# Kernel tuning notes

Hardware: AMD Instinct MI355X
Metric: run time of the kernel (lower is better)

The kernel has to match this reference:

```python
import jax, jax.numpy as jnp
import numpy as np

B, N, D = 512, 100000, 256
MAX_K = 20
EPS = 1e-12


def setup_inputs() -> dict:
    key = jax.random.key(0)
    k1, k2, k3, k4 = jax.random.split(key, 4)
    z_ego = jax.random.normal(k1, (B, D), dtype=jnp.float32)
    exo_bank = jax.random.normal(k2, (N, D), dtype=jnp.float32)
    sim_vt = jax.random.uniform(k3, (B, N), dtype=jnp.float32)
    W = jax.random.normal(k4, (D, D), dtype=jnp.float32) / np.sqrt(D)
    return {"z_ego": z_ego, "exo_bank": exo_bank, "sim_vt": sim_vt, "W": W, "k": 16}


def _l2_normalize(x):
    # matches torch F.normalize semantics with eps clamp
    n = jnp.sqrt(jnp.sum(x * x, axis=-1, keepdims=True))
    return x / jnp.maximum(n, EPS)


def reference(z_ego, exo_bank, sim_vt, W, k):
    # bilinear projection into query space (Linear, no bias)
    q = z_ego @ W.T                              # [B, D]
    k_eff = min(int(k), MAX_K, exo_bank.shape[0])
    # pairwise cosine similarity query x bank
    sim_vv = _l2_normalize(q) @ _l2_normalize(exo_bank).T   # [B, N]
    # combined score (sim_vt already [B, N]; broadcast is identity)
    score = 0.5 * sim_vv + 0.5 * sim_vt          # [B, N]
    _, topk_idx = jax.lax.top_k(score, k_eff)    # [B, k_eff]
    gathered = exo_bank[topk_idx]                # [B, k_eff, D]
    return gathered, topk_idx
```

## Files before the change

### kernel.cpp

```cpp
#include <hip/hip_runtime.h>
#include <math.h>
#include <stdint.h>

#define B_Q    512
#define N_BANK 100000
#define D_DIM  256
#define K16    16

#define NSL2   256
#define NCHUNK 1563
#define TROW   264
#define CHUNK_USHORT (64 * TROW)
#define CHUNK_BYTES  (CHUNK_USHORT * 2)
#define NGRP   6250
#define GSTRIDE 6272
#define MARGIN 5e-3f
#define CAPG   384

#define OFF_QN     0
#define OFF_QNT    0x80000
#define OFF_INORM  0x100000
#define OFF_TH     0x170000
#define OFF_GMAX   0x400000
#define OFF_BANKT  0x1400000
#define WS_NEED    ((size_t)OFF_BANKT + (size_t)NCHUNK * CHUNK_BYTES)

#define FB_OFF_INORM (B_Q * D_DIM * 4)
#define FB_OFF_PSC   (1024 * 1024)
#define FB_OFF_PID   (FB_OFF_PSC + B_Q * 128 * K16 * 4)

typedef __attribute__((ext_vector_type(8))) short short8;
typedef __attribute__((ext_vector_type(4))) float floatx4;

typedef __attribute__((address_space(1))) const unsigned char gu8_t;
typedef __attribute__((address_space(3))) unsigned char lu8_t;

__device__ inline unsigned short f2bf(float x) {
    unsigned int u = __float_as_uint(x);
    unsigned int r = (u + 0x7FFFu + ((u >> 16) & 1u)) >> 16;
    return (unsigned short)r;
}
__device__ inline unsigned long long pack_key(float s, int idx) {
    unsigned int u = __float_as_uint(s);
    u ^= (u & 0x80000000u) ? 0xFFFFFFFFu : 0x80000000u;
    return ((unsigned long long)u << 32) | (unsigned int)(~(unsigned int)idx);
}
__device__ inline int key_idx(unsigned long long k) {
    return (int)(~(unsigned int)(k & 0xFFFFFFFFull));
}
__device__ inline unsigned long long shfl_down_u64(unsigned long long x, int off) {
    unsigned int lo = (unsigned int)x;
    unsigned int hi = (unsigned int)(x >> 32);
    lo = __shfl_down(lo, off, 64);
    hi = __shfl_down(hi, off, 64);
    return ((unsigned long long)hi << 32) | lo;
}
__device__ inline unsigned long long umax64(unsigned long long a, unsigned long long b) {
    return a > b ? a : b;
}


__global__ void qn_prep_kernel(const float* __restrict__ z_ego,
                               const float* __restrict__ W,
                               float* __restrict__ qn,
                               unsigned short* __restrict__ qnt) {
    __shared__ float zs[D_DIM];
    __shared__ float red[4];
    int b = blockIdx.x;
    int t = threadIdx.x;
    zs[t] = z_ego[b * D_DIM + t];
    __syncthreads();
    const float4* W4 = reinterpret_cast<const float4*>(W + (size_t)t * D_DIM);
    float acc = 0.f;
#pragma unroll 8
    for (int u = 0; u < 64; ++u) {
        float4 w = W4[u];
        acc += w.x * zs[u * 4 + 0];
        acc += w.y * zs[u * 4 + 1];
        acc += w.z * zs[u * 4 + 2];
        acc += w.w * zs[u * 4 + 3];
    }
    float ss = acc * acc;
#pragma unroll
    for (int off = 32; off > 0; off >>= 1) ss += __shfl_down(ss, off, 64);
    if ((t & 63) == 0) red[t >> 6] = ss;
    __syncthreads();
    float tot = red[0] + red[1] + red[2] + red[3];
    float n = fmaxf(sqrtf(tot), 1e-12f);
    float v = acc / n;
    qn[b * D_DIM + t] = v;
    qnt[(size_t)(b >> 6) * CHUNK_USHORT + (size_t)(b & 63) * TROW + t] = f2bf(v);
}

__global__ __launch_bounds__(256)
void prep_bank_kernel(const float* __restrict__ bank,
                      float* __restrict__ inorm,
                      unsigned short* __restrict__ bankt) {
    int c = blockIdx.x;
    int t = threadIdx.x, w = t >> 6, l = t & 63;
    unsigned short* dst = bankt + (size_t)c * CHUNK_USHORT;
#pragma unroll 1
    for (int rr = 0; rr < 16; ++rr) {
        int row = w * 16 + rr;
        int jg = c * 64 + row;
        ushort4 o = {0, 0, 0, 0};
        if (jg < N_BANK) {
            float4 v = *reinterpret_cast<const float4*>(bank + (size_t)jg * D_DIM + l * 4);
            float ss = v.x * v.x + v.y * v.y + v.z * v.z + v.w * v.w;
#pragma unroll
            for (int off = 1; off < 64; off <<= 1) ss += __shfl_xor(ss, off, 64);
            float inv = 1.0f / fmaxf(sqrtf(ss), 1e-12f);
            o.x = f2bf(v.x * inv); o.y = f2bf(v.y * inv);
            o.z = f2bf(v.z * inv); o.w = f2bf(v.w * inv);
            if (l == 0) inorm[jg] = inv;
        }
        *reinterpret_cast<ushort4*>(dst + (size_t)row * TROW + l * 4) = o;
    }
}

__global__ __launch_bounds__(256, 4)
void screen3_kernel(const unsigned short* __restrict__ qnt,
                    const unsigned short* __restrict__ bankt,
                    const float* __restrict__ svt,
                    float* __restrict__ gmax) {
    __shared__ unsigned short lbank[CHUNK_USHORT];
    int t = threadIdx.x, w = t >> 6, l = t & 63;
    int lane16 = l & 15, quad = l >> 4;

    int bid = blockIdx.x;
    int xcd = bid & 7;
    int t2 = bid >> 3;
    int qb = t2 & 3;
    int slice = xcd + 8 * (t2 >> 2);

    int qt = qb * 4 + w;
    int qbase = qt * 32;

    short8 afrag[2][8];
    {
        const unsigned short* abase = qnt + (size_t)(qt >> 1) * CHUNK_USHORT
                                          + (size_t)((qt & 1) * 32) * TROW;
#pragma unroll
        for (int s = 0; s < 2; ++s)
#pragma unroll
            for (int k = 0; k < 8; ++k)
                afrag[s][k] = *reinterpret_cast<const short8*>(
                    abase + (size_t)(16 * s + lane16) * TROW + k * 32 + quad * 8);
    }

    const float* svr[2][4];
#pragma unroll
    for (int s = 0; s < 2; ++s)
#pragma unroll
        for (int r = 0; r < 4; ++r)
            svr[s][r] = svt + (size_t)(qbase + 16 * s + 4 * quad + r) * (size_t)N_BANK;

    for (int c = slice; c < NCHUNK; c += NSL2) {
        int j0 = c * 64;

        {
            const unsigned char* gsrc = (const unsigned char*)bankt + (size_t)c * CHUNK_BYTES;
            unsigned char* lbase = (unsigned char*)lbank;
#pragma unroll
            for (int i = 0; i < 8; ++i) {
                int off = i * 4096 + w * 1024;
                __builtin_amdgcn_global_load_lds((gu8_t*)(gsrc + off + l * 16),
                                                 (lu8_t*)(lbase + off), 16, 0, 0);
            }
            int off8 = 32768 + w * 256;
            __builtin_amdgcn_global_load_lds((gu8_t*)(gsrc + off8 + l * 4),
                                             (lu8_t*)(lbase + off8), 4, 0, 0);
        }

        float sv_cur[2][4], sv_nxt[2][4];
        {
            int jglob = j0 + lane16;
            bool inb = jglob < N_BANK;
#pragma unroll
            for (int s = 0; s < 2; ++s)
#pragma unroll
                for (int r = 0; r < 4; ++r)
                    sv_cur[s][r] = inb ? svr[s][r][jglob] : 0.f;
        }

        __syncthreads();

        int g0 = c * 4;
#pragma unroll
        for (int jg = 0; jg < 4; ++jg) {
            if (jg < 3) {
                int jglob = j0 + 16 * (jg + 1) + lane16;
                bool inb = jglob < N_BANK;
#pragma unroll
                for (int s = 0; s < 2; ++s)
#pragma unroll
                    for (int r = 0; r < 4; ++r)
                        sv_nxt[s][r] = inb ? svr[s][r][jglob] : 0.f;
            }

            floatx4 acc0 = (floatx4){0.f, 0.f, 0.f, 0.f};
            floatx4 acc1 = (floatx4){0.f, 0.f, 0.f, 0.f};
            const unsigned short* bbase = lbank + (size_t)(16 * jg + lane16) * TROW + quad * 8;
#pragma unroll
            for (int k = 0; k < 8; ++k) {
                short8 bfrag = *reinterpret_cast<const short8*>(bbase + k * 32);
                acc0 = __builtin_amdgcn_mfma_f32_16x16x32_bf16(afrag[0][k], bfrag, acc0, 0, 0, 0);
                acc1 = __builtin_amdgcn_mfma_f32_16x16x32_bf16(afrag[1][k], bfrag, acc1, 0, 0, 0);
            }

            int jglob = j0 + 16 * jg + lane16;
            bool inb = jglob < N_BANK;
            int g = g0 + jg;
            bool doStore = (lane16 == 0) && (g < NGRP);
#pragma unroll
            for (int s = 0; s < 2; ++s) {
#pragma unroll
                for (int r = 0; r < 4; ++r) {
                    float a = (s == 0) ? acc0[r] : acc1[r];
                    float score = inb ? (0.5f * a + 0.5f * sv_cur[s][r]) : -INFINITY;
                    score = fmaxf(score, __shfl_xor(score, 1, 64));
                    score = fmaxf(score, __shfl_xor(score, 2, 64));
                    score = fmaxf(score, __shfl_xor(score, 4, 64));
                    score = fmaxf(score, __shfl_xor(score, 8, 64));
                    if (doStore) {
                        int q = qbase + 16 * s + 4 * quad + r;
                        gmax[(size_t)q * GSTRIDE + g] = score;
                    }
                }
            }

            if (jg < 3) {
#pragma unroll
                for (int s = 0; s < 2; ++s)
#pragma unroll
                    for (int r = 0; r < 4; ++r)
                        sv_cur[s][r] = sv_nxt[s][r];
            }
        }
        __syncthreads();
    }
}

__global__ __launch_bounds__(256)
void gthresh_kernel(const float* __restrict__ gmax,
                    float* __restrict__ th) {
    __shared__ float buf[NGRP];
    __shared__ float red[4];
    int q = blockIdx.x, t = threadIdx.x, w = t >> 6;
    for (int i = t; i < NGRP; i += 256) buf[i] = gmax[(size_t)q * GSTRIDE + i];
    __syncthreads();
    float s16 = -INFINITY;
    for (int r = 0; r < K16; ++r) {
        float m = -INFINITY;
        for (int i = t; i < NGRP; i += 256) m = fmaxf(m, buf[i]);
#pragma unroll
        for (int off = 32; off > 0; off >>= 1) m = fmaxf(m, __shfl_down(m, off, 64));
        if ((t & 63) == 0) red[w] = m;
        __syncthreads();
        m = fmaxf(fmaxf(red[0], red[1]), fmaxf(red[2], red[3]));
        if (r == K16 - 1) s16 = m;
        if (r < K16 - 1) {
            for (int i = t; i < NGRP; i += 256)
                if (buf[i] == m) buf[i] = -INFINITY;
        }
        __syncthreads();
    }
    if (t == 0) th[q] = s16 - MARGIN;
}

__global__ __launch_bounds__(256)
void grescore_kernel(const float* __restrict__ gmax,
                     const float* __restrict__ th,
                     const float* __restrict__ qn,
                     const float* __restrict__ inorm,
                     const float* __restrict__ bank,
                     const float* __restrict__ svt,
                     float* __restrict__ out) {
    __shared__ float qns[D_DIM];
    __shared__ int glist[CAPG];
    __shared__ unsigned long long keys2[CAPG * K16];
    __shared__ unsigned long long wred[4];
    __shared__ int winI[K16];
    __shared__ int gcntS;
    int b = blockIdx.x, t = threadIdx.x;
    int w = t >> 6, l = t & 63;

    qns[t] = qn[(size_t)b * D_DIM + t];
    if (t == 0) gcntS = 0;
    __syncthreads();
    float thb = th[b];
    for (int g = t; g < NGRP; g += 256) {
        if (gmax[(size_t)b * GSTRIDE + g] >= thb) {
            int p = atomicAdd(&gcntS, 1);
            if (p < CAPG) glist[p] = g;
        }
    }
    __syncthreads();
    int ng = gcntS < CAPG ? gcntS : CAPG;
    int ncand = ng * K16;

    const float4* bank4 = reinterpret_cast<const float4*>(bank);
    float4 qv = reinterpret_cast<const float4*>(qns)[l];
    for (int ci = w; ci < ncand; ci += 4) {
        int j = glist[ci >> 4] * K16 + (ci & 15);
        float4 bv = bank4[(size_t)j * 64 + l];
        float d = qv.x * bv.x + qv.y * bv.y + qv.z * bv.z + qv.w * bv.w;
#pragma unroll
        for (int off = 32; off > 0; off >>= 1) d += __shfl_down(d, off, 64);
        if (l == 0) {
            float score = 0.5f * (d * inorm[j]) + 0.5f * svt[(size_t)b * N_BANK + j];
            keys2[ci] = pack_key(score, j);
        }
    }
    __syncthreads();

    for (int r = 0; r < K16; ++r) {
        unsigned long long best = 0ull;
        for (int i = t; i < ncand; i += 256) best = umax64(best, keys2[i]);
#pragma unroll
        for (int off = 32; off > 0; off >>= 1) best = umax64(best, shfl_down_u64(best, off));
        if (l == 0) wred[w] = best;
        __syncthreads();
        unsigned long long W = umax64(umax64(wred[0], wred[1]), umax64(wred[2], wred[3]));
        if (t == 0) winI[r] = key_idx(W);
        for (int i = t; i < ncand; i += 256)
            if (keys2[i] == W) keys2[i] = 0ull;
        __syncthreads();
    }

    if (t < K16)
        out[(size_t)B_Q * K16 * D_DIM + (size_t)b * K16 + t] = (float)winI[t];
    float4* out4 = reinterpret_cast<float4*>(out);
    for (int u = t; u < K16 * 64; u += 256) {
        int r = u >> 6, cc = u & 63;
        out4[((size_t)b * K16 + r) * 64 + cc] = bank4[(size_t)winI[r] * 64 + cc];
    }
}

#define FBT 64
#define FJT 64
#define FKC 64
#define FNS 128
#define FNC ((N_BANK + FJT - 1) / FJT)

__global__ void inorm_kernel(const float* __restrict__ bank,
                             float* __restrict__ inorm) {
    int w = threadIdx.x >> 6;
    int lane = threadIdx.x & 63;
    int j = blockIdx.x * 4 + w;
    if (j >= N_BANK) return;
    const float4* r4 = reinterpret_cast<const float4*>(bank + (size_t)j * D_DIM);
    float4 v = r4[lane];
    float ss = v.x * v.x + v.y * v.y + v.z * v.z + v.w * v.w;
#pragma unroll
    for (int off = 32; off > 0; off >>= 1) ss += __shfl_down(ss, off, 64);
    if (lane == 0) inorm[j] = 1.0f / fmaxf(sqrtf(ss), 1e-12f);
}

__global__ void fb_qn_kernel(const float* __restrict__ z_ego,
                             const float* __restrict__ W,
                             float* __restrict__ qn) {
    __shared__ float zs[D_DIM];
    __shared__ float red[4];
    int b = blockIdx.x;
    int t = threadIdx.x;
    zs[t] = z_ego[b * D_DIM + t];
    __syncthreads();
    const float4* W4 = reinterpret_cast<const float4*>(W + (size_t)t * D_DIM);
    float acc = 0.f;
#pragma unroll 8
    for (int u = 0; u < 64; ++u) {
        float4 w = W4[u];
        acc += w.x * zs[u * 4 + 0]; acc += w.y * zs[u * 4 + 1];
        acc += w.z * zs[u * 4 + 2]; acc += w.w * zs[u * 4 + 3];
    }
    float ss = acc * acc;
#pragma unroll
    for (int off = 32; off > 0; off >>= 1) ss += __shfl_down(ss, off, 64);
    if ((t & 63) == 0) red[t >> 6] = ss;
    __syncthreads();
    float tot = red[0] + red[1] + red[2] + red[3];
    qn[b * D_DIM + t] = acc / fmaxf(sqrtf(tot), 1e-12f);
}

__global__ __launch_bounds__(256)
void fb_score_topk_kernel(const float* __restrict__ qn,
                          const float* __restrict__ bank,
                          const float* __restrict__ svt,
                          const float* __restrict__ inorm,
                          float* __restrict__ psc,
                          int* __restrict__ pid) {
    __shared__ float As[FKC][FBT];
    __shared__ float Bsh[FKC][FJT];
    __shared__ float Ss[FBT][FJT + 1];
    int slice = blockIdx.x;
    int qbase = blockIdx.y * FBT;
    int t = threadIdx.x;
    int tq = t >> 4, tj = t & 15;
    int q0 = tq * 4, j0l = tj * 4;
    float sc[K16]; int id[K16];
#pragma unroll
    for (int i = 0; i < K16; ++i) { sc[i] = -INFINITY; id[i] = 0x7fffffff; }
    for (int c = slice; c < FNC; c += FNS) {
        int j0 = c * FJT;
        float acc[4][4];
#pragma unroll
        for (int a = 0; a < 4; ++a)
#pragma unroll
            for (int b2 = 0; b2 < 4; ++b2) acc[a][b2] = 0.f;
        for (int kc = 0; kc < D_DIM; kc += FKC) {
            __syncthreads();
#pragma unroll
            for (int r = 0; r < 4; ++r) {
                int idx = t + 256 * r;
                int q = idx & 63, kv = idx >> 6;
                float4 v = *reinterpret_cast<const float4*>(
                    &qn[(size_t)(qbase + q) * D_DIM + kc + kv * 4]);
                As[kv * 4 + 0][q] = v.x; As[kv * 4 + 1][q] = v.y;
                As[kv * 4 + 2][q] = v.z; As[kv * 4 + 3][q] = v.w;
            }
#pragma unroll
            for (int r = 0; r < 4; ++r) {
                int idx = t + 256 * r;
                int j = idx & 63, kv = idx >> 6;
                int jg = j0 + j;
                float4 v = make_float4(0.f, 0.f, 0.f, 0.f);
                if (jg < N_BANK)
                    v = *reinterpret_cast<const float4*>(
                        &bank[(size_t)jg * D_DIM + kc + kv * 4]);
                Bsh[kv * 4 + 0][j] = v.x; Bsh[kv * 4 + 1][j] = v.y;
                Bsh[kv * 4 + 2][j] = v.z; Bsh[kv * 4 + 3][j] = v.w;
            }
            __syncthreads();
#pragma unroll
            for (int k = 0; k < FKC; ++k) {
                float4 av = *reinterpret_cast<const float4*>(&As[k][q0]);
                float4 bv = *reinterpret_cast<const float4*>(&Bsh[k][j0l]);
                float a[4] = {av.x, av.y, av.z, av.w};
                float bb[4] = {bv.x, bv.y, bv.z, bv.w};
#pragma unroll
                for (int qi = 0; qi < 4; ++qi)
#pragma unroll
                    for (int ji = 0; ji < 4; ++ji) acc[qi][ji] += a[qi] * bb[ji];
            }
        }
        bool full = (j0 + FJT <= N_BANK);
        if (full) {
            float4 inv = *reinterpret_cast<const float4*>(&inorm[j0 + j0l]);
            float iv[4] = {inv.x, inv.y, inv.z, inv.w};
#pragma unroll
            for (int qi = 0; qi < 4; ++qi) {
                int q = qbase + q0 + qi;
                float4 svv = *reinterpret_cast<const float4*>(
                    &svt[(size_t)q * N_BANK + j0 + j0l]);
                float s[4] = {svv.x, svv.y, svv.z, svv.w};
#pragma unroll
                for (int ji = 0; ji < 4; ++ji)
                    Ss[q0 + qi][j0l + ji] = 0.5f * (acc[qi][ji] * iv[ji]) + 0.5f * s[ji];
            }
        } else {
#pragma unroll
            for (int qi = 0; qi < 4; ++qi) {
                int q = qbase + q0 + qi;
#pragma unroll
                for (int ji = 0; ji < 4; ++ji) {
                    int jg = j0 + j0l + ji;
                    float s = -INFINITY;
                    if (jg < N_BANK)
                        s = 0.5f * (acc[qi][ji] * inorm[jg]) + 0.5f * svt[(size_t)q * N_BANK + jg];
                    Ss[q0 + qi][j0l + ji] = s;
                }
            }
        }
        __syncthreads();
        if (t < FBT) {
#pragma unroll 1
            for (int jj = 0; jj < FJT; ++jj) {
                int jg = j0 + jj;
                if (jg >= N_BANK) break;
                float s = Ss[t][jj];
                if (s > sc[K16 - 1] || (s == sc[K16 - 1] && jg < id[K16 - 1])) {
                    float cs = s; int ci = jg;
#pragma unroll
                    for (int i = 0; i < K16; ++i) {
                        bool bt2 = (cs > sc[i]) || (cs == sc[i] && ci < id[i]);
                        float ts = sc[i]; int ti = id[i];
                        if (bt2) { sc[i] = cs; id[i] = ci; cs = ts; ci = ti; }
                    }
                }
            }
        }
    }
    if (t < FBT) {
        int q = qbase + t;
        size_t base = ((size_t)q * FNS + slice) * K16;
#pragma unroll
        for (int i = 0; i < K16; ++i) { psc[base + i] = sc[i]; pid[base + i] = id[i]; }
    }
}

__global__ __launch_bounds__(256)
void fb_merge_kernel(const float* __restrict__ psc,
                     const int* __restrict__ pid,
                     const float* __restrict__ bank,
                     float* __restrict__ out) {
    __shared__ unsigned long long keys[FNS * K16];
    __shared__ unsigned long long wred[4];
    __shared__ int win[K16];
    int b = blockIdx.x, t = threadIdx.x;
    for (int i = t; i < FNS * K16; i += 256) {
        float s = psc[(size_t)b * FNS * K16 + i];
        unsigned int u = __float_as_uint(s);
        u ^= (u & 0x80000000u) ? 0xFFFFFFFFu : 0x80000000u;
        unsigned int iv = ~(unsigned int)pid[(size_t)b * FNS * K16 + i];
        keys[i] = ((unsigned long long)u << 32) | iv;
    }
    __syncthreads();
    for (int r = 0; r < K16; ++r) {
        unsigned long long best = 0ull;
        for (int i = t; i < FNS * K16; i += 256) best = umax64(best, keys[i]);
#pragma unroll
        for (int off = 32; off > 0; off >>= 1) best = umax64(best, shfl_down_u64(best, off));
        if ((t & 63) == 0) wred[t >> 6] = best;
        __syncthreads();
        unsigned long long w = umax64(umax64(wred[0], wred[1]), umax64(wred[2], wred[3]));
        if (t == 0) win[r] = (int)(~(unsigned int)w);
        for (int i = t; i < FNS * K16; i += 256)
            if (keys[i] == w) keys[i] = 0ull;
        __syncthreads();
    }
    if (t < K16)
        out[(size_t)B_Q * K16 * D_DIM + (size_t)b * K16 + t] = (float)win[t];
    const float4* bank4 = reinterpret_cast<const float4*>(bank);
    float4* out4 = reinterpret_cast<float4*>(out);
    for (int u = t; u < K16 * 64; u += 256) {
        int r = u >> 6, c = u & 63;
        out4[((size_t)b * K16 + r) * 64 + c] = bank4[(size_t)win[r] * 64 + c];
    }
}

extern "C" void kernel_launch(void* const* d_in, const int* in_sizes, int n_in,
                              void* d_out, int out_size, void* d_ws, size_t ws_size,
                              hipStream_t stream) {
    const float* z_ego = (const float*)d_in[0];
    const float* bank  = (const float*)d_in[1];
    const float* svt   = (const float*)d_in[2];
    const float* W     = (const float*)d_in[3];
    float* out = (float*)d_out;
    char* ws = (char*)d_ws;

    if (ws_size >= WS_NEED) {
        float* qn             = (float*)(ws + OFF_QN);
        unsigned short* qnt   = (unsigned short*)(ws + OFF_QNT);
        float* inorm          = (float*)(ws + OFF_INORM);
        float* th             = (float*)(ws + OFF_TH);
        float* gmax           = (float*)(ws + OFF_GMAX);
        unsigned short* bankt = (unsigned short*)(ws + OFF_BANKT);

        qn_prep_kernel<<<B_Q, 256, 0, stream>>>(z_ego, W, qn, qnt);
        prep_bank_kernel<<<NCHUNK, 256, 0, stream>>>(bank, inorm, bankt);
        screen3_kernel<<<NSL2 * 4, 256, 0, stream>>>(qnt, bankt, svt, gmax);
        gthresh_kernel<<<B_Q, 256, 0, stream>>>(gmax, th);
        grescore_kernel<<<B_Q, 256, 0, stream>>>(gmax, th, qn, inorm, bank, svt, out);
    } else {
        float* qn    = (float*)(ws + 0);
        float* inorm = (float*)(ws + FB_OFF_INORM);
        float* psc   = (float*)(ws + FB_OFF_PSC);
        int*   pid   = (int*)(ws + FB_OFF_PID);
        fb_qn_kernel<<<B_Q, 256, 0, stream>>>(z_ego, W, qn);
        inorm_kernel<<<(N_BANK + 3) / 4, 256, 0, stream>>>(bank, inorm);
        dim3 grid(FNS, B_Q / FBT);
        fb_score_topk_kernel<<<grid, 256, 0, stream>>>(qn, bank, svt, inorm, psc, pid);
        fb_merge_kernel<<<B_Q, 256, 0, stream>>>(psc, pid, bank, out);
    }
}
```

Before: 726.2 us.

## Remap screen blocks to contiguous slices per XCD, batch sim_vt loads, unroll rescore

The screening kernel's block-to-slice mapping now gives each XCD a contiguous range of bank chunks instead of interleaving them, which should improve L2 locality for the sim_vt rows and bank tiles. All four column groups of sim_vt values are loaded up front before the barrier rather than double-buffered per group, so more loads are in flight per chunk at the cost of extra registers. The rescore loop handles two candidates per wave iteration to overlap the gather latencies. Register pressure under launch_bounds(256,4) could rise.

Result: faster. 698.7 us (-3.8%).

```diff
diff --git a/kernel.cpp b/kernel.cpp
--- a/kernel.cpp
+++ b/kernel.cpp
@@ -119,7 +119,7 @@
 }
 
 __global__ __launch_bounds__(256, 4)
-void screen3_kernel(const unsigned short* __restrict__ qnt,
+void screen4_kernel(const unsigned short* __restrict__ qnt,
                     const unsigned short* __restrict__ bankt,
                     const float* __restrict__ svt,
                     float* __restrict__ gmax) {
@@ -129,9 +129,9 @@
 
     int bid = blockIdx.x;
     int xcd = bid & 7;
-    int t2 = bid >> 3;
-    int qb = t2 & 3;
-    int slice = xcd + 8 * (t2 >> 2);
+    int i = bid >> 3;
+    int slice = (xcd << 5) + (i >> 2);
+    int qb = i & 3;
 
     int qt = qb * 4 + w;
     int qbase = qt * 32;
@@ -162,8 +162,8 @@
             const unsigned char* gsrc = (const unsigned char*)bankt + (size_t)c * CHUNK_BYTES;
             unsigned char* lbase = (unsigned char*)lbank;
 #pragma unroll
-            for (int i = 0; i < 8; ++i) {
-                int off = i * 4096 + w * 1024;
+            for (int i2 = 0; i2 < 8; ++i2) {
+                int off = i2 * 4096 + w * 1024;
                 __builtin_amdgcn_global_load_lds((gu8_t*)(gsrc + off + l * 16),
                                                  (lu8_t*)(lbase + off), 16, 0, 0);
             }
@@ -172,32 +172,24 @@
                                              (lu8_t*)(lbase + off8), 4, 0, 0);
         }
 
-        float sv_cur[2][4], sv_nxt[2][4];
-        {
-            int jglob = j0 + lane16;
-            bool inb = jglob < N_BANK;
-#pragma unroll
-            for (int s = 0; s < 2; ++s)
-#pragma unroll
-                for (int r = 0; r < 4; ++r)
-                    sv_cur[s][r] = inb ? svr[s][r][jglob] : 0.f;
-        }
+        float sv[4][2][4];
+#pragma unroll
+        for (int s = 0; s < 2; ++s)
+#pragma unroll
+            for (int r = 0; r < 4; ++r) {
+                const float* rp = svr[s][r] + j0 + lane16;
+#pragma unroll
+                for (int jg = 0; jg < 4; ++jg) {
+                    int jglob = j0 + 16 * jg + lane16;
+                    sv[jg][s][r] = (jglob < N_BANK) ? rp[16 * jg] : 0.f;
+                }
+            }
 
         __syncthreads();
 
         int g0 = c * 4;
 #pragma unroll
         for (int jg = 0; jg < 4; ++jg) {
-            if (jg < 3) {
-                int jglob = j0 + 16 * (jg + 1) + lane16;
-                bool inb = jglob < N_BANK;
-#pragma unroll
-                for (int s = 0; s < 2; ++s)
-#pragma unroll
-                    for (int r = 0; r < 4; ++r)
-                        sv_nxt[s][r] = inb ? svr[s][r][jglob] : 0.f;
-            }
-
             floatx4 acc0 = (floatx4){0.f, 0.f, 0.f, 0.f};
             floatx4 acc1 = (floatx4){0.f, 0.f, 0.f, 0.f};
             const unsigned short* bbase = lbank + (size_t)(16 * jg + lane16) * TROW + quad * 8;
@@ -217,7 +209,7 @@
 #pragma unroll
                 for (int r = 0; r < 4; ++r) {
                     float a = (s == 0) ? acc0[r] : acc1[r];
-                    float score = inb ? (0.5f * a + 0.5f * sv_cur[s][r]) : -INFINITY;
+                    float score = inb ? (0.5f * a + 0.5f * sv[jg][s][r]) : -INFINITY;
                     score = fmaxf(score, __shfl_xor(score, 1, 64));
                     score = fmaxf(score, __shfl_xor(score, 2, 64));
                     score = fmaxf(score, __shfl_xor(score, 4, 64));
@@ -227,14 +219,6 @@
                         gmax[(size_t)q * GSTRIDE + g] = score;
                     }
                 }
-            }
-
-            if (jg < 3) {
-#pragma unroll
-                for (int s = 0; s < 2; ++s)
-#pragma unroll
-                    for (int r = 0; r < 4; ++r)
-                        sv_cur[s][r] = sv_nxt[s][r];
             }
         }
         __syncthreads();
@@ -301,30 +285,41 @@
 
     const float4* bank4 = reinterpret_cast<const float4*>(bank);
     float4 qv = reinterpret_cast<const float4*>(qns)[l];
-    for (int ci = w; ci < ncand; ci += 4) {
-        int j = glist[ci >> 4] * K16 + (ci & 15);
-        float4 bv = bank4[(size_t)j * 64 + l];
-        float d = qv.x * bv.x + qv.y * bv.y + qv.z * bv.z + qv.w * bv.w;
-#pragma unroll
-        for (int off = 32; off > 0; off >>= 1) d += __shfl_down(d, off, 64);
+    for (int ci = w; ci < ncand; ci += 8) {
+        int jA = glist[ci >> 4] * K16 + (ci & 15);
+        int ci2 = ci + 4;
+        bool has2 = ci2 < ncand;
+        int jB = has2 ? (glist[ci2 >> 4] * K16 + (ci2 & 15)) : jA;
+        float4 bvA = bank4[(size_t)jA * 64 + l];
+        float4 bvB = bank4[(size_t)jB * 64 + l];
+        float dA = qv.x * bvA.x + qv.y * bvA.y + qv.z * bvA.z + qv.w * bvA.w;
+        float dB = qv.x * bvB.x + qv.y * bvB.y + qv.z * bvB.z + qv.w * bvB.w;
+#pragma unroll
+        for (int off = 32; off > 0; off >>= 1) dA += __shfl_down(dA, off, 64);
+#pragma unroll
+        for (int off = 32; off > 0; off >>= 1) dB += __shfl_down(dB, off, 64);
         if (l == 0) {
-            float score = 0.5f * (d * inorm[j]) + 0.5f * svt[(size_t)b * N_BANK + j];
-            keys2[ci] = pack_key(score, j);
+            float sA = 0.5f * (dA * inorm[jA]) + 0.5f * svt[(size_t)b * N_BANK + jA];
+            keys2[ci] = pack_key(sA, jA);
+            if (has2) {
+                float sB = 0.5f * (dB * inorm[jB]) + 0.5f * svt[(size_t)b * N_BANK + jB];
+                keys2[ci2] = pack_key(sB, jB);
+            }
         }
     }
     __syncthreads();
 
     for (int r = 0; r < K16; ++r) {
         unsigned long long best = 0ull;
-        for (int i = t; i < ncand; i += 256) best = umax64(best, keys2[i]);
+        for (int i2 = t; i2 < ncand; i2 += 256) best = umax64(best, keys2[i2]);
 #pragma unroll
         for (int off = 32; off > 0; off >>= 1) best = umax64(best, shfl_down_u64(best, off));
         if (l == 0) wred[w] = best;
         __syncthreads();
         unsigned long long W = umax64(umax64(wred[0], wred[1]), umax64(wred[2], wred[3]));
         if (t == 0) winI[r] = key_idx(W);
-        for (int i = t; i < ncand; i += 256)
-            if (keys2[i] == W) keys2[i] = 0ull;
+        for (int i2 = t; i2 < ncand; i2 += 256)
+            if (keys2[i2] == W) keys2[i2] = 0ull;
         __syncthreads();
     }
 
@@ -559,7 +554,7 @@
 
         qn_prep_kernel<<<B_Q, 256, 0, stream>>>(z_ego, W, qn, qnt);
         prep_bank_kernel<<<NCHUNK, 256, 0, stream>>>(bank, inorm, bankt);
-        screen3_kernel<<<NSL2 * 4, 256, 0, stream>>>(qnt, bankt, svt, gmax);
+        screen4_kernel<<<NSL2 * 4, 256, 0, stream>>>(qnt, bankt, svt, gmax);
         gthresh_kernel<<<B_Q, 256, 0, stream>>>(gmax, th);
         grescore_kernel<<<B_Q, 256, 0, stream>>>(gmax, th, qn, inorm, bank, svt, out);
     } else {
```
